# Kernel optimization log

Hardware: AMD Instinct MI355X
Metric: run time of the kernel (lower is better)

Reference implementation:

```python
import jax, jax.numpy as jnp
import numpy as np

N = 100000   # nodes
E = 1600000  # edges
D = 128      # input_dim
H = 128      # hidden_dim
CH = 16      # cluster_hidden_dim
P = 10       # processor_nodes


def setup_inputs() -> dict:
    key = jax.random.key(0)
    ks = jax.random.split(key, 22)
    s = 0.05
    return {
        "x": jax.random.normal(ks[0], (N, D), jnp.float32),
        "edges": jax.random.randint(ks[1], (2, E), 0, N, dtype=jnp.int32),
        "edge_attr": jax.random.uniform(ks[2], (E,), jnp.float32),
        "ready": jax.random.randint(ks[3], (N, 1), 0, 2, dtype=jnp.int32),
        "proc_emb": jax.random.normal(ks[4], (P, 3), jnp.float32),
        # GCN layers (PyG GCNConv: lin without bias, explicit bias added after aggregation)
        "gcn_w": jax.random.normal(ks[5], (2, D, H), jnp.float32) * s,
        "gcn_b": jax.random.normal(ks[6], (2, H), jnp.float32) * s,
        # listmlp: Linear(H,H) -> relu, then Linear(H,1)
        "mlp_w1": jax.random.normal(ks[7], (H, H), jnp.float32) * s,
        "mlp_b1": jax.random.normal(ks[8], (H,), jnp.float32) * s,
        "mlp_w2": jax.random.normal(ks[9], (H, 1), jnp.float32) * s,
        "mlp_b2": jax.random.normal(ks[10], (1,), jnp.float32) * s,
        # listmlp_value: Linear(H,1)
        "val_w": jax.random.normal(ks[11], (H, 1), jnp.float32) * s,
        "val_b": jax.random.normal(ks[12], (1,), jnp.float32) * s,
        # cluster_linear: Linear(3*P, CH)
        "cl_w": jax.random.normal(ks[13], (3 * P, CH), jnp.float32) * s,
        "cl_b": jax.random.normal(ks[14], (CH,), jnp.float32) * s,
        # listmlp_pass: Linear(H+CH,H) -> relu, then Linear(H,1)
        "pass_w1": jax.random.normal(ks[15], (H + CH, H), jnp.float32) * s,
        "pass_b1": jax.random.normal(ks[16], (H,), jnp.float32) * s,
        "pass_w2": jax.random.normal(ks[17], (H, 1), jnp.float32) * s,
        "pass_b2": jax.random.normal(ks[18], (1,), jnp.float32) * s,
    }


def _gcn_layer(x, row, col, w_e, W, b):
    # PyG GCNConv with flow='target_to_source': out[row] += norm_e * (x @ W)[col]
    # gcn_norm with idx=row: deg[i] = sum of edge weights with row==i (self-loops included)
    h = x @ W                                              # [N,H]
    deg = jax.ops.segment_sum(w_e, row, num_segments=N)    # [N]
    dis = jnp.where(deg > 0, jax.lax.rsqrt(deg), 0.0)      # deg^-1/2, inf -> 0
    norm = dis[row] * w_e * dis[col]                       # [E+N]
    msg = h[col] * norm[:, None]                           # [E+N,H] gather
    out = jax.ops.segment_sum(msg, row, num_segments=N)    # [N,H] scatter-add
    return out + b


def _forward(x, edges, edge_attr, ready, proc_emb, gcn_w, gcn_b,
             mlp_w1, mlp_b1, mlp_w2, mlp_b2, val_w, val_b, cl_w, cl_b,
             pass_w1, pass_b1, pass_w2, pass_b2):
    # add self-loops with weight 1 (GCNConv default add_self_loops=True)
    loop = jnp.arange(N, dtype=edges.dtype)
    row = jnp.concatenate([edges[0], loop])
    col = jnp.concatenate([edges[1], loop])
    w_e = jnp.concatenate([edge_attr, jnp.ones((N,), edge_attr.dtype)])

    h = x
    for l in range(2):
        h = jax.nn.relu(_gcn_layer(h, row, col, w_e, gcn_w[l], gcn_b[l]))

    mask = ready[:, 0] > 0                                 # [N] bool
    v = jnp.mean(h, axis=0)                                # [H]
    x_pass = jnp.max(jnp.where(mask[:, None], h, -jnp.inf), axis=0)  # masked max, [H]

    fc = proc_emb.reshape(-1) @ cl_w + cl_b                # [CH]
    x_pass = jnp.concatenate([x_pass, fc], axis=0)         # [H+CH]

    v = v @ val_w + val_b                                  # [1]

    logits = jax.nn.relu(h @ mlp_w1 + mlp_b1) @ mlp_w2 + mlp_b2        # [N,1]
    x_pass = jax.nn.relu(x_pass @ pass_w1 + pass_b1) @ pass_w2 + pass_b2  # [1]

    # torch indexes logits[ready]; here we mask non-ready entries with -inf so
    # the softmax over [N+1] matches torch's values on the ready rows.
    node_logits = jnp.where(mask, logits[:, 0], -jnp.inf)
    probs = jax.nn.softmax(jnp.concatenate([node_logits, x_pass], axis=0))  # [N+1]
    return probs, v


def reference(x, edges, edge_attr, ready, proc_emb, gcn_w, gcn_b,
              mlp_w1, mlp_b1, mlp_w2, mlp_b2, val_w, val_b, cl_w, cl_b,
              pass_w1, pass_b1, pass_w2, pass_b2):
    return _forward(x, edges, edge_attr, ready, proc_emb, gcn_w, gcn_b,
                    mlp_w1, mlp_b1, mlp_w2, mlp_b2, val_w, val_b, cl_w, cl_b,
                    pass_w1, pass_b1, pass_w2, pass_b2)
```

## Files before the change

kernel.cpp:

```cpp
#include <hip/hip_runtime.h>
#include <cstdint>

#define NN 100000
#define EE 1600000
#define HH 128
#define NREP 8
#define PSZ (NN / 8)
#define HPP (PSZ / 2)
#define SS 64
#define CAP 300000
#define NBB 500
#define BCH 3200
#define SCAN_CHUNK 512
#define NSCAN ((NN + SCAN_CHUNK - 1) / SCAN_CHUNK)

typedef unsigned long long u64;
typedef unsigned short ushort;
typedef unsigned char uchar;
typedef __attribute__((ext_vector_type(8))) short bf16x8;
typedef __attribute__((ext_vector_type(4))) float f32x4;
typedef __attribute__((ext_vector_type(2))) float f32x2;

__device__ __forceinline__ ushort f2bf(float x) {
    union { float f; unsigned u; } v; v.f = x;
    unsigned r = v.u + 0x7fffu + ((v.u >> 16) & 1u);
    return (ushort)(r >> 16);
}
__device__ __forceinline__ float bf2f(unsigned h16) {
    union { unsigned u; float f; } v; v.u = h16 << 16; return v.f;
}

__device__ __forceinline__ uchar f2fp8(float a) {
    return (uchar)(__builtin_amdgcn_cvt_pk_fp8_f32(a, a, 0, false) & 0xff);
}
__device__ __forceinline__ void unpack8_fp8(uint2 q, float* v) {
    f32x2 a = __builtin_amdgcn_cvt_pk_f32_fp8(q.x, false);
    f32x2 b = __builtin_amdgcn_cvt_pk_f32_fp8(q.x, true);
    f32x2 c = __builtin_amdgcn_cvt_pk_f32_fp8(q.y, false);
    f32x2 d = __builtin_amdgcn_cvt_pk_f32_fp8(q.y, true);
    v[0] = a[0]; v[1] = a[1]; v[2] = b[0]; v[3] = b[1];
    v[4] = c[0]; v[5] = c[1]; v[6] = d[0]; v[7] = d[1];
}

__device__ __forceinline__ unsigned encf(float f) {
    int b = __float_as_int(f);
    return (b >= 0) ? ((unsigned)b | 0x80000000u) : ~(unsigned)b;
}
__device__ __forceinline__ float decf(unsigned u) {
    return (u & 0x80000000u) ? __int_as_float((int)(u & 0x7fffffffu))
                             : __int_as_float((int)(~u));
}
#define ENC_NEG_INF 0x007FFFFFu

__global__ void k_setup(float* __restrict__ meansum, unsigned* __restrict__ maxenc,
                        unsigned* __restrict__ lmaxenc, float* __restrict__ esum,
                        int* __restrict__ gtail,
                        const float* __restrict__ w0, const float* __restrict__ w1,
                        const float* __restrict__ w2, ushort* __restrict__ wt) {
    int idx = blockIdx.x * blockDim.x + threadIdx.x;
    if (idx < NREP * HH) { meansum[idx] = 0.f; maxenc[idx] = ENC_NEG_INF; }
    if (idx < 8) gtail[idx] = 0;
    if (idx == 0) { lmaxenc[0] = ENC_NEG_INF; esum[0] = 0.f; }
    if (idx < 3 * HH * HH) {
        int mat = idx >> 14;
        int e = idx & 16383;
        int n = e >> 7, k = e & 127;
        const float* src = (mat == 0) ? w0 : (mat == 1) ? w1 : w2;
        wt[idx] = f2bf(src[k * HH + n]);
    }
}

__global__ __launch_bounds__(256) void k_bucket(const int* __restrict__ rows,
                                                const int* __restrict__ cols,
                                                const float* __restrict__ ea,
                                                int* __restrict__ gtail,
                                                u64* __restrict__ ebuck) {
    __shared__ u64 buf[8][1024];
    __shared__ int cnt8[8];
    __shared__ int rsv[8];
    int t = threadIdx.x;
    if (t < 8) cnt8[t] = 0;
    __syncthreads();
    int e0 = blockIdx.x * BCH;
    int e1 = e0 + BCH;
    for (int ebase = e0; ebase < e1; ebase += 1024) {
        int e = ebase + t * 4;
        if (e < e1) {
            int4 r4 = *(const int4*)(rows + e);
            int4 c4 = *(const int4*)(cols + e);
            float4 a4 = *(const float4*)(ea + e);
            int rr[4] = {r4.x, r4.y, r4.z, r4.w};
            int cc[4] = {c4.x, c4.y, c4.z, c4.w};
            float aa[4] = {a4.x, a4.y, a4.z, a4.w};
#pragma unroll
            for (int j = 0; j < 4; ++j) {
                int p = rr[j] / PSZ;
                int rl = rr[j] - p * PSZ;
                unsigned q = (unsigned)(aa[j] * 32767.0f + 0.5f);
                u64 en = ((u64)rl << 32) | (u64)(((unsigned)cc[j] << 15) | q);
                int idx = atomicAdd(&cnt8[p], 1);
                buf[p][idx] = en;
            }
        }
        __syncthreads();
        if (t < 8) rsv[t] = atomicAdd(&gtail[t], cnt8[t]);
        __syncthreads();
#pragma unroll
        for (int p = 0; p < 8; ++p) {
            int nn = cnt8[p], oo = rsv[p];
            u64* dst = ebuck + (size_t)p * CAP + oo;
            for (int j = t; j < nn; j += 256) dst[j] = buf[p][j];
        }
        __syncthreads();
        if (t < 8) cnt8[t] = 0;
        __syncthreads();
    }
}

__global__ __launch_bounds__(256) void k_cnt2(const u64* __restrict__ ebuck,
                                              const int* __restrict__ gtail,
                                              unsigned* __restrict__ cntp) {
    __shared__ unsigned h32[HPP];
    int b = blockIdx.x;
    int s = b >> 3, p = b & 7;
    for (int j = threadIdx.x; j < HPP; j += 256) h32[j] = 0;
    __syncthreads();
    int pc = gtail[p];
    int len = (pc + SS - 1) / SS;
    int lo = s * len, hi = min(lo + len, pc);
    const u64* src = ebuck + (size_t)p * CAP;
    for (int i = lo + threadIdx.x; i < hi; i += 256) {
        int rl = (int)(src[i] >> 32);
        atomicAdd(&h32[rl >> 1], (rl & 1) ? 0x10000u : 1u);
    }
    __syncthreads();
    unsigned* dst = cntp + (size_t)(p * SS + s) * HPP;
    for (int j = threadIdx.x; j < HPP; j += 256) dst[j] = h32[j];
}

__global__ void k_cntscan(const unsigned* __restrict__ cntp, int* __restrict__ count,
                          unsigned* __restrict__ deltap, int* __restrict__ basep,
                          int* __restrict__ bsum) {
    int b = blockIdx.x, t = threadIdx.x;
    int rp = b * 256 + t;
    int c0 = 0, c1 = 0;
    if (rp < NN / 2) {
        int p = rp / HPP, j = rp - p * HPP;
        unsigned s0 = 0, s1 = 0;
#pragma unroll 8
        for (int c = 0; c < SS; ++c) {
            size_t o = (size_t)(p * SS + c) * HPP + j;
            unsigned v = cntp[o];
            deltap[o] = s0 | (s1 << 16);
            s0 += v & 0xffffu;
            s1 += v >> 16;
        }
        c0 = (int)s0; c1 = (int)s1;
        *(int2*)(count + 2 * rp) = make_int2(c0, c1);
    }
    c0 = (c0 + 7) & ~7;
    c1 = (c1 + 7) & ~7;
    int s = c0 + c1;
    int lane = t & 63, w = t >> 6;
    int v = s;
#pragma unroll
    for (int off = 1; off < 64; off <<= 1) {
        int u = __shfl_up(v, off, 64);
        if (lane >= off) v += u;
    }
    __shared__ int wsum[4];
    if (lane == 63) wsum[w] = v;
    __syncthreads();
    int wadd = 0;
    for (int j = 0; j < w; ++j) wadd += wsum[j];
    int incl = v + wadd;
    int excl = incl - s;
    int i0 = 2 * rp;
    if (i0 < NN) basep[i0] = excl;
    if (i0 + 1 < NN) basep[i0 + 1] = excl + c0;
    if (t == 255) bsum[b] = incl;
}

__global__ void k_scan2(int* __restrict__ bsum, int* __restrict__ base) {
    __shared__ int tmp[256];
    int t = threadIdx.x;
    int v = (t < NSCAN) ? bsum[t] : 0;
    tmp[t] = v;
    __syncthreads();
    for (int off = 1; off < 256; off <<= 1) {
        int u = (t >= off) ? tmp[t - off] : 0;
        __syncthreads();
        tmp[t] += u;
        __syncthreads();
    }
    if (t == NSCAN - 1) base[NN] = tmp[t];
    if (t < NSCAN) bsum[t] = tmp[t] - v;
}

__global__ __launch_bounds__(256) void k_fill2(const u64* __restrict__ ebuck,
                                               const int* __restrict__ gtail,
                                               const unsigned* __restrict__ deltap,
                                               const int* __restrict__ basep,
                                               const int* __restrict__ bsum,
                                               unsigned* __restrict__ csre) {
    __shared__ int nxt[PSZ];
    int b = blockIdx.x;
    int s = b >> 3, p = b & 7;
    const unsigned* dsrc = deltap + (size_t)(p * SS + s) * HPP;
    const int* bsrc = basep + p * PSZ;
    for (int j = threadIdx.x; j < HPP; j += 256) {
        unsigned d = dsrc[j];
        int2 bb = *(const int2*)(bsrc + 2 * j);
        int badd = bsum[(p * PSZ + 2 * j) >> 9];
        nxt[2 * j] = bb.x + badd + (int)(d & 0xffffu);
        nxt[2 * j + 1] = bb.y + badd + (int)(d >> 16);
    }
    __syncthreads();
    int pc = gtail[p];
    int len = (pc + SS - 1) / SS;
    int lo = s * len, hi = min(lo + len, pc);
    const u64* src = ebuck + (size_t)p * CAP;
    for (int i = lo + threadIdx.x; i < hi; i += 256) {
        u64 en = src[i];
        int rl = (int)(en >> 32);
        int slot = atomicAdd(&nxt[rl], 1);
        csre[slot] = (unsigned)(en & 0xffffffffu);
    }
}

__global__ void k_degsum(const int* __restrict__ count, unsigned* __restrict__ csre,
                         const int* __restrict__ basep, const int* __restrict__ bsum,
                         int* __restrict__ base, float* __restrict__ dis) {
    int r = blockIdx.x * blockDim.x + threadIdx.x;
    if (r >= NN) return;
    int lo = basep[r] + bsum[r >> 9];
    int hip = (r == NN - 1) ? base[NN] : (basep[r + 1] + bsum[(r + 1) >> 9]);
    base[r] = lo;
    int hireal = lo + count[r];
    float s = 0.f;
    for (int e = lo; e < hireal; ++e) s += (float)(csre[e] & 0x7fffu);
    unsigned selfv = (unsigned)r << 15;
    for (int e = hireal; e < hip; ++e) csre[e] = selfv;
    dis[r] = rsqrtf(1.0f + s * (1.0f / 32767.0f));
}

__global__ __launch_bounds__(256) void k_gather(const uchar* __restrict__ hW,
                                                const unsigned* __restrict__ csre,
                                                const int* __restrict__ base,
                                                const float* __restrict__ dis,
                                                const float* __restrict__ bias,
                                                ushort* __restrict__ agg) {
    int node = blockIdx.x * 16 + (threadIdx.x >> 4);
    if (node >= NN) return;
    int l = threadIdx.x & 15;
    int f = l * 8;
    int lo = base[node], hi = base[node + 1];
    float disn = dis[node];
    float wk = disn * (1.0f / 32767.0f);
    float acc[8];
    {
        uint2 q = *(const uint2*)(hW + (size_t)node * HH + f);
        float v[8]; unpack8_fp8(q, v);
#pragma unroll
        for (int j = 0; j < 8; ++j) acc[j] = disn * v[j];
    }
    for (int eb = lo; eb < hi; eb += 8) {
        uint4 pa = *(const uint4*)(csre + eb);
        uint4 pb = *(const uint4*)(csre + eb + 4);
        unsigned pp[8] = {pa.x, pa.y, pa.z, pa.w, pb.x, pb.y, pb.z, pb.w};
        uint2 qq[8];
#pragma unroll
        for (int j = 0; j < 8; ++j)
            qq[j] = *(const uint2*)(hW + (size_t)(pp[j] >> 15) * HH + f);
#pragma unroll
        for (int j = 0; j < 8; ++j) {
            float w = (float)(pp[j] & 0x7fffu) * wk;
            float v[8]; unpack8_fp8(qq[j], v);
#pragma unroll
            for (int k = 0; k < 8; ++k) acc[k] += w * v[k];
        }
    }
    float4 b0 = *(const float4*)(bias + f);
    float4 b1 = *(const float4*)(bias + f + 4);
    ushort o[8];
    o[0] = f2bf(acc[0] + b0.x); o[1] = f2bf(acc[1] + b0.y);
    o[2] = f2bf(acc[2] + b0.z); o[3] = f2bf(acc[3] + b0.w);
    o[4] = f2bf(acc[4] + b1.x); o[5] = f2bf(acc[5] + b1.y);
    o[6] = f2bf(acc[6] + b1.z); o[7] = f2bf(acc[7] + b1.w);
    *(uint4*)(agg + (size_t)node * HH + f) = *(uint4*)o;
}

template <int MODE>
__global__ __launch_bounds__(256) void k_mfma(const void* __restrict__ Ain,
                                              const ushort* __restrict__ Wt,
                                              uchar* __restrict__ C,
                                              const float* __restrict__ dis,
                                              const float* __restrict__ b1,
                                              const float* __restrict__ w2v,
                                              const float* __restrict__ b2,
                                              const int* __restrict__ ready,
                                              float* __restrict__ logits,
                                              float* __restrict__ meansum,
                                              unsigned* __restrict__ maxenc,
                                              unsigned* __restrict__ lmaxenc, int n) {
    __shared__ ushort As[64 * HH];
    __shared__ ushort Ws[128 * HH];
    __shared__ int rdy[64];
    __shared__ unsigned slmax;
    const int t = threadIdx.x;
    const int rb = blockIdx.x * 64;
    if (MODE == 2) {
        if (t < 64) rdy[t] = (rb + t < n) ? ready[rb + t] : 0;
        if (t == 0) slmax = ENC_NEG_INF;
    }
#pragma unroll
    for (int i = 0; i < 8; ++i) {
        int nr = i * 16 + (t >> 4);
        int gc = t & 15;
        uint4 q = *(const uint4*)(Wt + (size_t)nr * HH + gc * 8);
        *(uint4*)(Ws + nr * HH + ((gc ^ (nr & 15)) * 8)) = q;
    }
#pragma unroll
    for (int i = 0; i < 4; ++i) {
        int m = i * 16 + (t >> 4);
        int k = (t & 15) * 8;
        ushort pk[8];
        if (MODE == 0) {
            const float* Af = (const float*)Ain;
            float4 v0 = make_float4(0.f, 0.f, 0.f, 0.f), v1 = v0;
            if (rb + m < n) {
                const float* src = Af + (size_t)(rb + m) * HH + k;
                v0 = *(const float4*)src;
                v1 = *(const float4*)(src + 4);
            }
            pk[0] = f2bf(v0.x); pk[1] = f2bf(v0.y); pk[2] = f2bf(v0.z); pk[3] = f2bf(v0.w);
            pk[4] = f2bf(v1.x); pk[5] = f2bf(v1.y); pk[6] = f2bf(v1.z); pk[7] = f2bf(v1.w);
        } else {
            const ushort* Au = (const ushort*)Ain;
            uint4 q = make_uint4(0, 0, 0, 0);
            if (rb + m < n) q = *(const uint4*)(Au + (size_t)(rb + m) * HH + k);
            *(uint4*)pk = q;
#pragma unroll
            for (int j = 0; j < 8; ++j) pk[j] = (pk[j] & 0x8000) ? (ushort)0 : pk[j];
        }
        int gsw = (t & 15) ^ (m & 15);
        *(uint4*)(As + m * HH + gsw * 8) = *(uint4*)pk;
    }
    __syncthreads();

    const int wave = t >> 6, lane = t & 63;
    const int cl = lane & 15;
    const int kq = lane >> 4;
    const int m0 = wave * 16;

    f32x4 acc[8];
#pragma unroll
    for (int c = 0; c < 8; ++c) acc[c] = (f32x4){0.f, 0.f, 0.f, 0.f};

#pragma unroll
    for (int kk = 0; kk < 4; ++kk) {
        int g = kk * 4 + kq;
        bf16x8 bfr = *(const bf16x8*)(As + (m0 + cl) * HH + ((g ^ cl) * 8));
#pragma unroll
        for (int c = 0; c < 8; ++c) {
            bf16x8 afr = *(const bf16x8*)(Ws + (c * 16 + cl) * HH + ((g ^ cl) * 8));
            acc[c] = __builtin_amdgcn_mfma_f32_16x16x32_bf16(afr, bfr, acc[c], 0, 0, 0);
        }
    }

    const int node = rb + m0 + cl;
    if (MODE < 2) {
        if (node < n) {
            float d = dis[node];
            uchar* dst = C + (size_t)node * HH + kq * 4;
#pragma unroll
            for (int c = 0; c < 8; ++c) {
                unsigned u = __builtin_amdgcn_cvt_pk_fp8_f32(acc[c][0] * d, acc[c][1] * d, 0u, false);
                u = __builtin_amdgcn_cvt_pk_fp8_f32(acc[c][2] * d, acc[c][3] * d, u, true);
                *(unsigned*)(dst + c * 16) = u;
            }
        }
    } else {
        float s = 0.f;
#pragma unroll
        for (int c = 0; c < 8; ++c) {
            float4 bb = *(const float4*)(b1 + c * 16 + kq * 4);
            float4 ww = *(const float4*)(w2v + c * 16 + kq * 4);
            s += fmaxf(acc[c][0] + bb.x, 0.f) * ww.x;
            s += fmaxf(acc[c][1] + bb.y, 0.f) * ww.y;
            s += fmaxf(acc[c][2] + bb.z, 0.f) * ww.z;
            s += fmaxf(acc[c][3] + bb.w, 0.f) * ww.w;
        }
        s += __shfl_xor(s, 16, 64);
        s += __shfl_xor(s, 32, 64);
        unsigned mylmax = ENC_NEG_INF;
        if (kq == 0 && node < n) {
            float lg = s + b2[0];
            logits[node] = lg;
            if (rdy[m0 + cl] > 0) mylmax = encf(lg);
        }
        if (mylmax != ENC_NEG_INF) atomicMax(&slmax, mylmax);

        int lim = min(64, n - rb);
        if (t < HH) {
            int f = t, gf = f >> 3, fo = f & 7;
            float sum = 0.f, mx = -3.4e38f;
            for (int m = 0; m < lim; ++m) {
                float v = bf2f(As[m * HH + ((gf ^ (m & 15)) * 8) + fo]);
                sum += v;
                if (rdy[m] > 0) mx = fmaxf(mx, v);
            }
            int rep = blockIdx.x & (NREP - 1);
            atomicAdd(&meansum[rep * HH + f], sum);
            if (mx > -3.0e38f) atomicMax(&maxenc[rep * HH + f], encf(mx));
        }
        __syncthreads();
        if (t == 0 && slmax != ENC_NEG_INF) atomicMax(lmaxenc, slmax);
    }
}

__global__ void k_fin1(const float* __restrict__ meansum, const unsigned* __restrict__ maxenc,
                       const unsigned* __restrict__ lmaxenc,
                       const float* __restrict__ val_w, const float* __restrict__ val_b,
                       const float* __restrict__ pe, const float* __restrict__ cl_w,
                       const float* __restrict__ cl_b, const float* __restrict__ pw1,
                       const float* __restrict__ pb1, const float* __restrict__ pw2,
                       const float* __restrict__ pb2, float* __restrict__ scal,
                       float* __restrict__ d_out) {
    __shared__ float xp[144];
    __shared__ float msum[HH];
    __shared__ float zp[HH];
    int t = threadIdx.x;
    if (t < HH) {
        float s = 0.f;
        unsigned mx = ENC_NEG_INF;
#pragma unroll
        for (int r = 0; r < NREP; ++r) {
            s += meansum[r * HH + t];
            unsigned e = maxenc[r * HH + t];
            if (e > mx) mx = e;
        }
        msum[t] = s;
        xp[t] = decf(mx);
    } else if (t < 144) {
        int c = t - HH;
        float s = cl_b[c];
        for (int k = 0; k < 30; ++k) s += pe[k] * cl_w[k * 16 + c];
        xp[t] = s;
    }
    __syncthreads();
    if (t < HH) {
        float s = pb1[t];
        for (int k = 0; k < 144; ++k) s += xp[k] * pw1[k * HH + t];
        zp[t] = fmaxf(s, 0.f);
    }
    __syncthreads();
    if (t < 64) {
        float s1 = zp[t] * pw2[t] + zp[t + 64] * pw2[t + 64];
        float s2 = msum[t] * val_w[t] + msum[t + 64] * val_w[t + 64];
#pragma unroll
        for (int off = 32; off > 0; off >>= 1) {
            s1 += __shfl_xor(s1, off, 64);
            s2 += __shfl_xor(s2, off, 64);
        }
        if (t == 0) {
            float xpass = s1 + pb2[0];
            float v = s2 * (1.0f / NN) + val_b[0];
            float M = fmaxf(decf(lmaxenc[0]), xpass);
            scal[0] = M;
            scal[1] = expf(xpass - M);
            d_out[NN + 1] = v;
        }
    }
}

__global__ __launch_bounds__(256) void k_exp(const float* __restrict__ logits,
                                             const int* __restrict__ ready,
                                             const float* __restrict__ scal,
                                             float* __restrict__ d_out,
                                             float* __restrict__ esum) {
    __shared__ float warr[4];
    int t = threadIdx.x;
    int i = blockIdx.x * 256 + t;
    float M = scal[0];
    float p = 0.f;
    if (i < NN) {
        if (ready[i] > 0) p = expf(logits[i] - M);
        d_out[i] = p;
    }
    float s = p;
#pragma unroll
    for (int off = 32; off > 0; off >>= 1) s += __shfl_xor(s, off, 64);
    if ((t & 63) == 0) warr[t >> 6] = s;
    __syncthreads();
    if (t == 0) atomicAdd(esum, warr[0] + warr[1] + warr[2] + warr[3]);
}

__global__ void k_scale(const float* __restrict__ esum, const float* __restrict__ scal,
                        float* __restrict__ d_out) {
    int i = blockIdx.x * blockDim.x + threadIdx.x;
    float inv = 1.0f / (esum[0] + scal[1]);
    if (i < NN) d_out[i] *= inv;
    else if (i == NN) d_out[NN] = scal[1] * inv;
}

extern "C" void kernel_launch(void* const* d_in, const int* in_sizes, int n_in,
                              void* d_out, int out_size, void* d_ws, size_t ws_size,
                              hipStream_t stream) {
    const float* x      = (const float*)d_in[0];
    const int*   edges  = (const int*)d_in[1];
    const float* eattr  = (const float*)d_in[2];
    const int*   ready  = (const int*)d_in[3];
    const float* pe     = (const float*)d_in[4];
    const float* gcn_w  = (const float*)d_in[5];
    const float* gcn_b  = (const float*)d_in[6];
    const float* mlp_w1 = (const float*)d_in[7];
    const float* mlp_b1 = (const float*)d_in[8];
    const float* mlp_w2 = (const float*)d_in[9];
    const float* mlp_b2 = (const float*)d_in[10];
    const float* val_w  = (const float*)d_in[11];
    const float* val_b  = (const float*)d_in[12];
    const float* cl_w   = (const float*)d_in[13];
    const float* cl_b   = (const float*)d_in[14];
    const float* pw1    = (const float*)d_in[15];
    const float* pb1    = (const float*)d_in[16];
    const float* pw2    = (const float*)d_in[17];
    const float* pb2    = (const float*)d_in[18];

    const int* rows = edges;
    const int* cols = edges + EE;

    char* P = (char*)d_ws;
    size_t off = 0;
    auto carve = [&](size_t bytes) {
        off = (off + 255) & ~(size_t)255;
        void* p = P + off;
        off += bytes;
        return p;
    };
    float* dis     = (float*)carve(NN * 4);
    float* logits  = (float*)carve(NN * 4);
    int*   count   = (int*)carve(NN * 4);
    int*   basep   = (int*)carve(NN * 4);
    int*   base    = (int*)carve((NN + 1) * 4);
    int*   bsum    = (int*)carve(256 * 4);
    ushort* bufB   = (ushort*)carve((size_t)NN * HH * 2);
    uchar* bufH    = (uchar*)carve((size_t)NN * HH);
    unsigned* csre = (unsigned*)carve((size_t)(EE + 8 * NN) * 4);
    u64*   ebuck   = (u64*)carve((size_t)8 * CAP * 8);
    float* meansum = (float*)carve(NREP * HH * 4);
    unsigned* maxenc = (unsigned*)carve(NREP * HH * 4);
    unsigned* lmaxenc = (unsigned*)carve(4);
    float* esum    = (float*)carve(4);
    float* scal    = (float*)carve(8);
    int*   gtail   = (int*)carve(8 * 4);
    ushort* wt     = (ushort*)carve(3 * HH * HH * 2);

    unsigned* cntp   = (unsigned*)bufB;
    unsigned* deltap = (unsigned*)bufB + (size_t)8 * SS * HPP;

    float* out = (float*)d_out;

    const int nb = (NN + 255) / 256;
    const int gb = (NN + 63) / 64;
    const int ab = (NN + 15) / 16;
    const int pb = 8 * SS;

    k_setup<<<(3 * HH * HH + 255) / 256, 256, 0, stream>>>(meansum, maxenc, lmaxenc, esum,
                                                           gtail, gcn_w, gcn_w + HH * HH,
                                                           mlp_w1, wt);

    k_bucket<<<NBB, 256, 0, stream>>>(rows, cols, eattr, gtail, ebuck);
    k_cnt2<<<pb, 256, 0, stream>>>(ebuck, gtail, cntp);
    k_cntscan<<<NSCAN, 256, 0, stream>>>(cntp, count, deltap, basep, bsum);
    k_scan2<<<1, 256, 0, stream>>>(bsum, base);
    k_fill2<<<pb, 256, 0, stream>>>(ebuck, gtail, deltap, basep, bsum, csre);
    k_degsum<<<nb, 256, 0, stream>>>(count, csre, basep, bsum, base, dis);

    k_mfma<0><<<gb, 256, 0, stream>>>(x, wt, bufH, dis, nullptr, nullptr, nullptr, nullptr,
                                      nullptr, nullptr, nullptr, nullptr, NN);
    k_gather<<<ab, 256, 0, stream>>>(bufH, csre, base, dis, gcn_b, bufB);

    k_mfma<1><<<gb, 256, 0, stream>>>(bufB, wt + HH * HH, bufH, dis, nullptr, nullptr, nullptr,
                                      nullptr, nullptr, nullptr, nullptr, nullptr, NN);
    k_gather<<<ab, 256, 0, stream>>>(bufH, csre, base, dis, gcn_b + HH, bufB);

    k_mfma<2><<<gb, 256, 0, stream>>>(bufB, wt + 2 * HH * HH, nullptr, nullptr, mlp_b1, mlp_w2,
                                      mlp_b2, ready, logits, meansum, maxenc, lmaxenc, NN);
    k_fin1<<<1, 256, 0, stream>>>(meansum, maxenc, lmaxenc, val_w, val_b, pe, cl_w, cl_b,
                                  pw1, pb1, pw2, pb2, scal, out);
    k_exp<<<nb, 256, 0, stream>>>(logits, ready, scal, out, esum);
    k_scale<<<(NN + 1 + 255) / 256, 256, 0, stream>>>(esum, scal, out);
}
```

Baseline: 341.2 us.

## Pre-swizzle weights and aggregates for direct global-to-LDS loads in MFMA kernel

```diff
diff --git a/kernel.cpp b/kernel.cpp
--- a/kernel.cpp
+++ b/kernel.cpp
@@ -20,6 +20,16 @@
 typedef __attribute__((ext_vector_type(8))) short bf16x8;
 typedef __attribute__((ext_vector_type(4))) float f32x4;
 typedef __attribute__((ext_vector_type(2))) float f32x2;
+
+__device__ __forceinline__ void gl2lds16(const void* g, void* l) {
+#if __has_builtin(__builtin_amdgcn_global_load_lds)
+    __builtin_amdgcn_global_load_lds(
+        (const __attribute__((address_space(1))) unsigned int*)g,
+        (__attribute__((address_space(3))) unsigned int*)l, 16, 0, 0);
+#else
+    *(uint4*)l = *(const uint4*)g;
+#endif
+}
 
 __device__ __forceinline__ ushort f2bf(float x) {
     union { float f; unsigned u; } v; v.f = x;
@@ -65,8 +75,10 @@
         int mat = idx >> 14;
         int e = idx & 16383;
         int n = e >> 7, k = e & 127;
+        int g = k >> 3, el = k & 7;
         const float* src = (mat == 0) ? w0 : (mat == 1) ? w1 : w2;
-        wt[idx] = f2bf(src[k * HH + n]);
+        int pos = (mat << 14) | (n << 7) | (((g ^ (n & 15)) << 3) | el);
+        wt[pos] = f2bf(src[k * HH + n]);
     }
 }
 
@@ -283,11 +295,12 @@
     float4 b0 = *(const float4*)(bias + f);
     float4 b1 = *(const float4*)(bias + f + 4);
     ushort o[8];
-    o[0] = f2bf(acc[0] + b0.x); o[1] = f2bf(acc[1] + b0.y);
-    o[2] = f2bf(acc[2] + b0.z); o[3] = f2bf(acc[3] + b0.w);
-    o[4] = f2bf(acc[4] + b1.x); o[5] = f2bf(acc[5] + b1.y);
-    o[6] = f2bf(acc[6] + b1.z); o[7] = f2bf(acc[7] + b1.w);
-    *(uint4*)(agg + (size_t)node * HH + f) = *(uint4*)o;
+    o[0] = f2bf(fmaxf(acc[0] + b0.x, 0.f)); o[1] = f2bf(fmaxf(acc[1] + b0.y, 0.f));
+    o[2] = f2bf(fmaxf(acc[2] + b0.z, 0.f)); o[3] = f2bf(fmaxf(acc[3] + b0.w, 0.f));
+    o[4] = f2bf(fmaxf(acc[4] + b1.x, 0.f)); o[5] = f2bf(fmaxf(acc[5] + b1.y, 0.f));
+    o[6] = f2bf(fmaxf(acc[6] + b1.z, 0.f)); o[7] = f2bf(fmaxf(acc[7] + b1.w, 0.f));
+    int gsw = (l ^ (node & 15)) * 8;
+    *(uint4*)(agg + (size_t)node * HH + gsw) = *(uint4*)o;
 }
 
 template <int MODE>
@@ -309,23 +322,31 @@
     __shared__ unsigned slmax;
     const int t = threadIdx.x;
     const int rb = blockIdx.x * 64;
-    if (MODE == 2) {
-        if (t < 64) rdy[t] = (rb + t < n) ? ready[rb + t] : 0;
-        if (t == 0) slmax = ENC_NEG_INF;
-    }
-#pragma unroll
-    for (int i = 0; i < 8; ++i) {
-        int nr = i * 16 + (t >> 4);
-        int gc = t & 15;
-        uint4 q = *(const uint4*)(Wt + (size_t)nr * HH + gc * 8);
-        *(uint4*)(Ws + nr * HH + ((gc ^ (nr & 15)) * 8)) = q;
-    }
-#pragma unroll
-    for (int i = 0; i < 4; ++i) {
-        int m = i * 16 + (t >> 4);
-        int k = (t & 15) * 8;
-        ushort pk[8];
-        if (MODE == 0) {
+    const int wv = t >> 6, ln = t & 63;
+
+    {
+        const char* wsb = (const char*)Wt;
+        char* wdb = (char*)Ws;
+#pragma unroll
+        for (int i = 0; i < 8; ++i) {
+            int blk = wv * 8 + i;
+            gl2lds16(wsb + blk * 1024 + ln * 16, wdb + blk * 1024);
+        }
+    }
+    if (MODE != 0) {
+        const char* asb = (const char*)Ain + (size_t)rb * HH * 2;
+        char* adb = (char*)As;
+#pragma unroll
+        for (int i = 0; i < 4; ++i) {
+            int blk = wv * 4 + i;
+            gl2lds16(asb + blk * 1024 + ln * 16, adb + blk * 1024);
+        }
+    } else {
+#pragma unroll
+        for (int i = 0; i < 4; ++i) {
+            int m = i * 16 + (t >> 4);
+            int k = (t & 15) * 8;
+            ushort pk[8];
             const float* Af = (const float*)Ain;
             float4 v0 = make_float4(0.f, 0.f, 0.f, 0.f), v1 = v0;
             if (rb + m < n) {
@@ -335,23 +356,19 @@
             }
             pk[0] = f2bf(v0.x); pk[1] = f2bf(v0.y); pk[2] = f2bf(v0.z); pk[3] = f2bf(v0.w);
             pk[4] = f2bf(v1.x); pk[5] = f2bf(v1.y); pk[6] = f2bf(v1.z); pk[7] = f2bf(v1.w);
-        } else {
-            const ushort* Au = (const ushort*)Ain;
-            uint4 q = make_uint4(0, 0, 0, 0);
-            if (rb + m < n) q = *(const uint4*)(Au + (size_t)(rb + m) * HH + k);
-            *(uint4*)pk = q;
-#pragma unroll
-            for (int j = 0; j < 8; ++j) pk[j] = (pk[j] & 0x8000) ? (ushort)0 : pk[j];
-        }
-        int gsw = (t & 15) ^ (m & 15);
-        *(uint4*)(As + m * HH + gsw * 8) = *(uint4*)pk;
-    }
-    __syncthreads();
-
-    const int wave = t >> 6, lane = t & 63;
-    const int cl = lane & 15;
-    const int kq = lane >> 4;
-    const int m0 = wave * 16;
+            int gsw = (t & 15) ^ (m & 15);
+            *(uint4*)(As + m * HH + gsw * 8) = *(uint4*)pk;
+        }
+    }
+    if (MODE == 2) {
+        if (t < 64) rdy[t] = (rb + t < n) ? ready[rb + t] : 0;
+        if (t == 0) slmax = ENC_NEG_INF;
+    }
+    __syncthreads();
+
+    const int cl = ln & 15;
+    const int kq = ln >> 4;
+    const int m0 = wv * 16;
 
     f32x4 acc[8];
 #pragma unroll
```

Result: no change. 335.2 us (-1.8%).
